# Optimization experiments

Hardware: AMD Instinct MI355X
Metric: run time of the kernel (lower is better)

The kernel has to match this reference:

```python
import jax, jax.numpy as jnp
import numpy as np

H = 256        # hidden_channels (== out_channels)
IN = 128       # in_channels (atom features)
ED = 64        # edge_dim (bond features)
G = 1024       # num graphs
L = 48         # atoms per graph (static pad length)
N = G * L      # num atoms
E = 2 * N      # num directed edges
NLAYERS = 4


def setup_inputs() -> dict:
    key = jax.random.key(0)
    ks = jax.random.split(key, 12)
    def rn(k, shape, scale=0.05):
        return jax.random.normal(k, shape, jnp.float32) * scale
    return {
        "x": jax.random.normal(ks[0], (N, IN), jnp.float32),
        "edge_attr": jax.random.normal(ks[1], (E, ED), jnp.float32),
        "edge_index": jax.random.randint(ks[2], (2, E), 0, N),
        "batch": jnp.repeat(jnp.arange(G), L),  # sorted, L atoms per graph
        "w_atom": rn(ks[3], (IN, H)), "b_atom": jnp.zeros((H,), jnp.float32),
        "w_bond": rn(ks[4], (ED, H)), "b_bond": jnp.zeros((H,), jnp.float32),
        "conv_w": rn(ks[5], (NLAYERS, H, H)), "conv_b": jnp.zeros((NLAYERS, H), jnp.float32),
        "w_lin": rn(ks[6], (3 * H, H)), "b_lin": jnp.zeros((H,), jnp.float32),
        "gru_bias": rn(ks[7], (H,), 0.06),
        "w_ih": rn(ks[8], (2, 3 * H, H)), "w_hh": rn(ks[9], (2, 3 * H, H)),
        "b_ih": jnp.zeros((2, 3 * H), jnp.float32), "b_hh": jnp.zeros((2, 3 * H), jnp.float32),
        "w_out": rn(ks[10], (2 * H, H)), "b_out": jnp.zeros((H,), jnp.float32),
    }


def reference(x, edge_attr, edge_index, batch, w_atom, b_atom, w_bond, b_bond,
              conv_w, conv_b, w_lin, b_lin, gru_bias, w_ih, w_hh, b_ih, b_hh,
              w_out, b_out):
    relu = jax.nn.relu
    row, col = edge_index[0], edge_index[1]  # flow='target_to_source': aggregate at row

    x_proj = relu(x @ w_atom + b_atom)                 # [N, H]
    h_atom = x_proj
    h_bond = relu(edge_attr @ w_bond + b_bond)         # [E, H]

    def booster(h_bond):
        # message_booster multi-aggregation: sum * max (empty slots -> 0, as torch_scatter)
        s = jax.ops.segment_sum(h_bond, row, num_segments=N)
        m = jax.ops.segment_max(h_bond, row, num_segments=N)
        m = jnp.where(jnp.isfinite(m), m, 0.0)
        return s * m

    for i in range(NLAYERS - 1):
        h_atom = h_atom + booster(h_bond)              # additive communicator
        # edge_update: x[edge_index_i] - edge_attr[edge_index_j]; seq = Linear+ReLU (dropout p=0)
        h_bond = relu((h_atom[row] - h_bond[col]) @ conv_w[i] + conv_b[i])
    aggr_message = h_atom + booster(h_bond)            # last conv; edge output discarded

    h = jnp.concatenate([aggr_message, h_atom, x_proj], axis=1) @ w_lin + b_lin  # [N, H]

    # ---- BatchGRU ----
    msg = relu(h + gru_bias)
    starts = jnp.searchsorted(batch, jnp.arange(G))
    pos = jnp.arange(N) - starts[batch]                # position within own graph
    messages = jnp.zeros((G, L, H), h.dtype).at[batch, pos].set(msg)
    h0 = jax.ops.segment_max(h, batch, num_segments=G)  # [G, H], same init both dirs

    def gru_dir(seq, d):
        def cell(hst, x_t):
            gi = x_t @ w_ih[d].T + b_ih[d]
            gh = hst @ w_hh[d].T + b_hh[d]
            i_r, i_z, i_n = jnp.split(gi, 3, -1)
            h_r, h_z, h_n = jnp.split(gh, 3, -1)
            r = jax.nn.sigmoid(i_r + h_r)
            z = jax.nn.sigmoid(i_z + h_z)
            n = jnp.tanh(i_n + r * h_n)
            hn = (1.0 - z) * n + z * hst
            return hn, hn
        _, out = jax.lax.scan(cell, h0, seq)
        return out

    seq = messages.transpose(1, 0, 2)                  # [L, G, H]
    out_f = gru_dir(seq, 0)
    out_b = gru_dir(seq[::-1], 1)[::-1]
    h_msgs = jnp.concatenate([out_f, out_b], -1).transpose(1, 0, 2)  # [G, L, 2H]
    unpadded = h_msgs[batch, pos]                      # [N, 2H]

    return relu(unpadded @ w_out + b_out)              # seq_out (dropout p=0)
```

## Files before the change

kernel.cpp:

```cpp
#include <hip/hip_runtime.h>
#include <math.h>

#define HH 256
#define GG 1024
#define LL 48
#define NNODES 49152
#define NEDGES 98304
#define SB 256.0f
#define DSB 0.00390625f

typedef _Float16 f16;
typedef __attribute__((ext_vector_type(8))) _Float16 f16x8;
typedef __attribute__((ext_vector_type(4))) float f32x4;

#define MFMA16(a, b, c) __builtin_amdgcn_mfma_f32_16x16x32_f16(a, b, c, 0, 0, 0)

__device__ inline float sc_from_max(float m) {
    if (!(m > 0.f)) return 1.0f;
    return ldexpf(1.0f, 13 - ilogbf(m));
}

__global__ void csr_count(const int* __restrict__ row, int* __restrict__ counts)
{
    int e = blockIdx.x * 256 + threadIdx.x;
    if (e < NEDGES) atomicAdd(&counts[row[e]], 1);
}

__global__ __launch_bounds__(1024) void scan_offsets(const int* __restrict__ counts,
                                                     int* __restrict__ offsets)
{
    __shared__ int tsum[1024];
    const int tid = threadIdx.x;
    const int base = tid * 48;
    int s = 0;
    for (int i = 0; i < 48; i++) s += counts[base + i];
    tsum[tid] = s;
    __syncthreads();
    for (int off = 1; off < 1024; off <<= 1) {
        int v = (tid >= off) ? tsum[tid - off] : 0;
        __syncthreads();
        tsum[tid] += v;
        __syncthreads();
    }
    int run = (tid == 0) ? 0 : tsum[tid - 1];
    for (int i = 0; i < 48; i++) { offsets[base + i] = run; run += counts[base + i]; }
    if (tid == 1023) offsets[NNODES] = run;
}

__global__ void csr_fill(const int* __restrict__ row, const int* __restrict__ offsets,
                         int* __restrict__ cursor, int* __restrict__ elist)
{
    int e = blockIdx.x * 256 + threadIdx.x;
    if (e < NEDGES) {
        int r = row[e];
        int p = atomicAdd(&cursor[r], 1);
        elist[offsets[r] + p] = e;
    }
}

__global__ void prep_graphs(const int* __restrict__ batch, int* __restrict__ starts,
                            int* __restrict__ gcnt)
{
    int i = blockIdx.x * 256 + threadIdx.x;
    if (i < NNODES) {
        int b = batch[i];
        atomicAdd(&gcnt[b], 1);
        if (i == 0 || batch[i - 1] != b) starts[b] = i;
    }
}

__global__ void rowscale(const float* __restrict__ A, int K, float* __restrict__ sc)
{
    int m = blockIdx.x, ln = threadIdx.x;
    float v = 0.f;
    for (int k = ln; k < K; k += 64) v = fmaxf(v, fabsf(A[(size_t)m * K + k]));
    for (int s = 32; s; s >>= 1) v = fmaxf(v, __shfl_xor(v, s));
    if (ln == 0) sc[m] = sc_from_max(v);
}

__global__ void prep_wT(const float* __restrict__ Wsrc, f16* __restrict__ oH,
                        f16* __restrict__ oL)
{
    int idx = blockIdx.x * 256 + threadIdx.x;
    int k = idx >> 8, n = idx & 255;
    float v = Wsrc[(size_t)k * 256 + n] * SB;
    f16 h = (f16)v;
    size_t o = ((size_t)(k >> 5) * 256 + n) * 32 + (k & 31);
    oH[o] = h;
    oL[o] = (f16)(v - (float)h);
}

__global__ void prep_gruW(const float* __restrict__ w_ih, const float* __restrict__ w_hh,
                          const float* __restrict__ b_ih, const float* __restrict__ b_hh,
                          f16* __restrict__ BgH, f16* __restrict__ BgL,
                          float* __restrict__ bias4)
{
    int idx = blockIdx.x * 256 + threadIdx.x;
    int d = idx >> 19;
    int rem = idx & 524287;
    int k = rem >> 10;
    int col = rem & 1023;
    int jj = col >> 2, s = col & 3;
    const float* Wi = w_ih + (size_t)d * 768 * 256;
    const float* Wh = w_hh + (size_t)d * 768 * 256;
    float v;
    if (s == 0)      v = (k < 256) ? Wi[(size_t)jj * 256 + k]         : Wh[(size_t)jj * 256 + (k - 256)];
    else if (s == 1) v = (k < 256) ? Wi[(size_t)(256 + jj) * 256 + k] : Wh[(size_t)(256 + jj) * 256 + (k - 256)];
    else if (s == 2) v = (k < 256) ? Wi[(size_t)(512 + jj) * 256 + k] : 0.f;
    else             v = (k < 256) ? 0.f : Wh[(size_t)(512 + jj) * 256 + (k - 256)];
    v *= SB;
    f16 h = (f16)v;
    size_t o = ((size_t)(d * 16 + (k >> 5)) * 1024 + col) * 32 + (k & 31);
    BgH[o] = h;
    BgL[o] = (f16)(v - (float)h);
    if (k == 0) {
        const float* bi = b_ih + d * 768;
        const float* bh = b_hh + d * 768;
        float bv;
        if (s == 0)      bv = bi[jj] + bh[jj];
        else if (s == 1) bv = bi[256 + jj] + bh[256 + jj];
        else if (s == 2) bv = bi[512 + jj];
        else             bv = bh[512 + jj];
        bias4[d * 1024 + col] = bv;
    }
}

__global__ void booster(const float* __restrict__ hb_lo, const float* __restrict__ hb_hi,
                        const float* __restrict__ atom_in, float* __restrict__ out,
                        const int* __restrict__ offsets, const int* __restrict__ elist,
                        float* __restrict__ scOut)
{
    int n = blockIdx.x, c = threadIdx.x;
    int b0 = offsets[n], b1 = offsets[n + 1];
    float s = 0.f, m = 0.f;
    for (int p = b0; p < b1; p++) {
        int e = elist[p];
        const float* hb = (e < NNODES) ? (hb_lo + (size_t)e * HH)
                                       : (hb_hi + (size_t)(e - NNODES) * HH);
        float v = hb[c];
        s += v;
        m = fmaxf(m, v);
    }
    float o = atom_in[(size_t)n * HH + c] + s * m;
    out[(size_t)n * HH + c] = o;
    float v = fabsf(o);
    for (int t = 32; t; t >>= 1) v = fmaxf(v, __shfl_xor(v, t));
    __shared__ float wm[4];
    if ((c & 63) == 0) wm[c >> 6] = v;
    __syncthreads();
    if (c == 0)
        scOut[n] = sc_from_max(fmaxf(fmaxf(wm[0], wm[1]), fmaxf(wm[2], wm[3])));
}

__global__ void h0_init(const float* __restrict__ h, const int* __restrict__ starts,
                        const int* __restrict__ gcnt, float* __restrict__ hid0,
                        float* __restrict__ scG)
{
    int g = blockIdx.x, c = threadIdx.x;
    int st = starts[g], cn = gcnt[g];
    float m = -INFINITY, am = 0.f;
    for (int i = 0; i < cn; i++) {
        float v = h[(size_t)(st + i) * HH + c];
        m = fmaxf(m, v);
        am = fmaxf(am, fabsf(v));
    }
    if (cn == 0) m = 0.f;
    hid0[(size_t)g * HH + c] = m;
    hid0[(size_t)GG * HH + (size_t)g * HH + c] = m;
    for (int t = 32; t; t >>= 1) am = fmaxf(am, __shfl_xor(am, t));
    __shared__ float wm[4];
    if ((c & 63) == 0) wm[c >> 6] = am;
    __syncthreads();
    if (c == 0) {
        float M = fmaxf(fmaxf(fmaxf(wm[0], wm[1]), fmaxf(wm[2], wm[3])) + 0.07f, 1.0f);
        scG[g] = sc_from_max(M);
    }
}

__global__ void build_msgP(const float* __restrict__ h, const float* __restrict__ gbias,
                           const int* __restrict__ starts, const int* __restrict__ gcnt,
                           float* __restrict__ msgP)
{
    int l = blockIdx.x, g = blockIdx.y, k = threadIdx.x;
    float v = 0.f;
    if (l < gcnt[g]) {
        int node = starts[g] + l;
        v = fmaxf(h[(size_t)node * HH + k] + gbias[k], 0.f);
    }
    msgP[((size_t)l * GG + g) * HH + k] = v;
}

template<int MODE>
__device__ __forceinline__ void gemmLoadA(const float* __restrict__ A,
    const float* __restrict__ S0, const float* __restrict__ S1,
    const float* __restrict__ S2, int rI, int cI, int row, int K, int k,
    float va[8])
{
    if constexpr (MODE == 0) {
        const float* p = A + (size_t)row * K + k;
        float4 v0 = *(const float4*)p, v1 = *(const float4*)(p + 4);
        va[0]=v0.x; va[1]=v0.y; va[2]=v0.z; va[3]=v0.w;
        va[4]=v1.x; va[5]=v1.y; va[6]=v1.z; va[7]=v1.w;
    } else if constexpr (MODE == 1) {
        const float* pa = S0 + (size_t)rI * HH + k;
        const float* pb = S1 + (size_t)cI * HH + k;
        float4 a0 = *(const float4*)pa, a1 = *(const float4*)(pa + 4);
        float4 b0 = *(const float4*)pb, b1 = *(const float4*)(pb + 4);
        va[0]=a0.x-b0.x; va[1]=a0.y-b0.y; va[2]=a0.z-b0.z; va[3]=a0.w-b0.w;
        va[4]=a1.x-b1.x; va[5]=a1.y-b1.y; va[6]=a1.z-b1.z; va[7]=a1.w-b1.w;
    } else if constexpr (MODE == 2) {
        const float* S = (k < 256) ? S0 : ((k < 512) ? S1 : S2);
        const float* p = S + (size_t)row * HH + (k & 255);
        float4 v0 = *(const float4*)p, v1 = *(const float4*)(p + 4);
        va[0]=v0.x; va[1]=v0.y; va[2]=v0.z; va[3]=v0.w;
        va[4]=v1.x; va[5]=v1.y; va[6]=v1.z; va[7]=v1.w;
    } else {
        const float* S = (k < 256) ? S0 : S1;
        const float* p = S + (size_t)row * HH + (k & 255);
        float4 v0 = *(const float4*)p, v1 = *(const float4*)(p + 4);
        va[0]=v0.x; va[1]=v0.y; va[2]=v0.z; va[3]=v0.w;
        va[4]=v1.x; va[5]=v1.y; va[6]=v1.z; va[7]=v1.w;
    }
}

template<int MODE, bool RELU, bool SPLITC, bool WSCALE, int NX>
__global__ __launch_bounds__(256) void gemm_f16x3(
    const float* __restrict__ A,
    const float* __restrict__ S0, const float* __restrict__ S1, const float* __restrict__ S2,
    const int* __restrict__ ridx, const int* __restrict__ cidx,
    const f16* __restrict__ BgH, const f16* __restrict__ BgL,
    const float* __restrict__ bias,
    const float* __restrict__ sc0, const float* __restrict__ sc1, const float* __restrict__ sc2,
    float* __restrict__ Clo, float* __restrict__ Chi,
    float* __restrict__ scOut, int K)
{
    __shared__ __align__(16) f16 Ah[64 * 40], Al[64 * 40];
    __shared__ __align__(16) f16 Bh[256 * 40], Bl[256 * 40];
    __shared__ float scL[64];
    __shared__ float rmL[64][4];

    const int tid = threadIdx.x;
    const int m0 = blockIdx.x * 64;
    const int arow = tid >> 2, aoct = tid & 3;
    const int w = tid >> 6, lane = tid & 63, lr = lane & 15, lh = lane >> 4;

    if (tid < 64) {
        float sc;
        if constexpr (MODE == 0) sc = sc0[m0 + tid];
        else if constexpr (MODE == 1) {
            int r = ridx[m0 + tid], cc = cidx[m0 + tid];
            sc = fminf(sc0[r], sc1[cc]) * 0.5f;
        } else if constexpr (MODE == 2) {
            sc = fminf(fminf(sc0[m0 + tid], sc1[m0 + tid]), sc2[m0 + tid]);
        } else {
            sc = sc0[cidx[m0 + tid]];
        }
        scL[tid] = sc;
    }
    int rI = 0, cI = 0;
    if constexpr (MODE == 1) { rI = ridx[m0 + arow]; cI = cidx[m0 + arow]; }
    __syncthreads();
    const float myS = scL[arow];

    float va[8];
    f16x8 rbh[4], rbl[4];
    gemmLoadA<MODE>(A, S0, S1, S2, rI, cI, m0 + arow, K, aoct * 8, va);
    {
        size_t base = (size_t)tid * 32;
        const f16x8* ph = (const f16x8*)(BgH + base);
#pragma unroll
        for (int q = 0; q < 4; q++) rbh[q] = ph[q];
        if constexpr (NX == 3) {
            const f16x8* pl = (const f16x8*)(BgL + base);
#pragma unroll
            for (int q = 0; q < 4; q++) rbl[q] = pl[q];
        }
    }

    f32x4 acc[4][4] = {};
    for (int k0 = 0; k0 < K; k0 += 32) {
        {
            f16x8 hi, lo;
#pragma unroll
            for (int e = 0; e < 8; e++) {
                float a = va[e] * myS;
                f16 h = (f16)a;
                hi[e] = h;
                if constexpr (NX == 3) lo[e] = (f16)(a - (float)h);
            }
            *(f16x8*)&Ah[arow * 40 + aoct * 8] = hi;
            if constexpr (NX == 3) *(f16x8*)&Al[arow * 40 + aoct * 8] = lo;
        }
#pragma unroll
        for (int q = 0; q < 4; q++) {
            *(f16x8*)&Bh[tid * 40 + q * 8] = rbh[q];
            if constexpr (NX == 3) *(f16x8*)&Bl[tid * 40 + q * 8] = rbl[q];
        }
        __syncthreads();
        if (k0 + 32 < K) {
            gemmLoadA<MODE>(A, S0, S1, S2, rI, cI, m0 + arow, K, k0 + 32 + aoct * 8, va);
            size_t base = ((size_t)((k0 + 32) >> 5) * 256 + tid) * 32;
            const f16x8* ph = (const f16x8*)(BgH + base);
#pragma unroll
            for (int q = 0; q < 4; q++) rbh[q] = ph[q];
            if constexpr (NX == 3) {
                const f16x8* pl = (const f16x8*)(BgL + base);
#pragma unroll
                for (int q = 0; q < 4; q++) rbl[q] = pl[q];
            }
        }
        f16x8 fah[4], fal[4];
#pragma unroll
        for (int i = 0; i < 4; i++) {
            fah[i] = *(const f16x8*)&Ah[(i * 16 + lr) * 40 + lh * 8];
            if constexpr (NX == 3) fal[i] = *(const f16x8*)&Al[(i * 16 + lr) * 40 + lh * 8];
        }
#pragma unroll
        for (int j = 0; j < 4; j++) {
            int colx = w * 64 + j * 16 + lr;
            f16x8 fbh = *(const f16x8*)&Bh[colx * 40 + lh * 8];
            if constexpr (NX == 3) {
                f16x8 fbl = *(const f16x8*)&Bl[colx * 40 + lh * 8];
#pragma unroll
                for (int i = 0; i < 4; i++) {
                    acc[i][j] = MFMA16(fah[i], fbh, acc[i][j]);
                    acc[i][j] = MFMA16(fah[i], fbl, acc[i][j]);
                    acc[i][j] = MFMA16(fal[i], fbh, acc[i][j]);
                }
            } else {
#pragma unroll
                for (int i = 0; i < 4; i++)
                    acc[i][j] = MFMA16(fah[i], fbh, acc[i][j]);
            }
        }
        __syncthreads();
    }

    float rm[4][4];
#pragma unroll
    for (int i = 0; i < 4; i++)
#pragma unroll
        for (int e = 0; e < 4; e++) rm[i][e] = 0.f;
#pragma unroll
    for (int i = 0; i < 4; i++) {
#pragma unroll
        for (int e = 0; e < 4; e++) {
            int ml = i * 16 + lh * 4 + e;
            int m = m0 + ml;
            float inv = DSB / scL[ml];
            float* Cb;
            if constexpr (SPLITC)
                Cb = (m < NNODES) ? (Clo + (size_t)m * HH) : (Chi + (size_t)(m - NNODES) * HH);
            else
                Cb = Clo + (size_t)m * HH;
#pragma unroll
            for (int j = 0; j < 4; j++) {
                int n = w * 64 + j * 16 + lr;
                float v = acc[i][j][e] * inv + bias[n];
                if constexpr (RELU) v = fmaxf(v, 0.f);
                Cb[n] = v;
                if constexpr (WSCALE) rm[i][e] = fmaxf(rm[i][e], fabsf(v));
            }
        }
    }
    if constexpr (WSCALE) {
#pragma unroll
        for (int i = 0; i < 4; i++)
#pragma unroll
            for (int e = 0; e < 4; e++) {
                float v = rm[i][e];
                v = fmaxf(v, __shfl_xor(v, 1));
                v = fmaxf(v, __shfl_xor(v, 2));
                v = fmaxf(v, __shfl_xor(v, 4));
                v = fmaxf(v, __shfl_xor(v, 8));
                if (lr == 0) rmL[i * 16 + lh * 4 + e][w] = v;
            }
        __syncthreads();
        if (tid < 64)
            scOut[m0 + tid] = sc_from_max(fmaxf(fmaxf(rmL[tid][0], rmL[tid][1]),
                                                fmaxf(rmL[tid][2], rmL[tid][3])));
    }
}

__global__ __launch_bounds__(256) void gru_step_f16(
    const float* __restrict__ msgP, const f16* __restrict__ BgH, const f16* __restrict__ BgL,
    const float* __restrict__ bias4, const float* __restrict__ hidC, float* __restrict__ hidN,
    const float* __restrict__ scG, const int* __restrict__ starts, const int* __restrict__ gcnt,
    float* __restrict__ outF, float* __restrict__ outB, int t)
{
    __shared__ __align__(16) char smemraw[18432];
    float* Cs = (float*)smemraw;
    __shared__ float scL[32];

    const int tid = threadIdx.x;
    const int id = blockIdx.x;
    const int c = id & 7, d = (id >> 3) & 1, gt = id >> 4;
    const int g0 = gt * 32;
    const int l = d ? (LL - 1 - t) : t;
    const float* hidCd = hidC + (size_t)d * GG * HH;
    float* hidNd = hidN + (size_t)d * GG * HH;

    if (tid < 32) scL[tid] = scG[g0 + tid];
    __syncthreads();

    const int arow = tid >> 3, akoct = tid & 7;
    const float myS = scL[arow];
    const int w = tid >> 6, lane = tid & 63, lr = lane & 15, lh = lane >> 4;

    f16* Ah0 = (f16*)smemraw;
    f16* Al0 = Ah0 + 2304;
    f16* Ah1 = Al0 + 2304;
    f16* Al1 = Ah1 + 2304;

    {
        const float* p = msgP + ((size_t)l * GG + g0 + arow) * HH + akoct * 8;
        float4 v0 = *(const float4*)p, v1 = *(const float4*)(p + 4);
        float va0[8] = {v0.x, v0.y, v0.z, v0.w, v1.x, v1.y, v1.z, v1.w};
        f16x8 hi, lo;
#pragma unroll
        for (int e = 0; e < 8; e++) {
            float a = va0[e] * myS;
            f16 h = (f16)a;
            hi[e] = h;
            lo[e] = (f16)(a - (float)h);
        }
        *(f16x8*)&Ah0[arow * 72 + akoct * 8] = hi;
        *(f16x8*)&Al0[arow * 72 + akoct * 8] = lo;
    }
    f16x8 fbh[2][2], fbl[2][2];
#pragma unroll
    for (int ks = 0; ks < 2; ks++) {
        size_t kbase = (size_t)(d * 16 + ks) * 1024;
#pragma unroll
        for (int j = 0; j < 2; j++) {
            size_t o = (kbase + (c * 128 + w * 32 + j * 16 + lr)) * 32 + lh * 8;
            fbh[ks][j] = *(const f16x8*)(BgH + o);
            fbl[ks][j] = *(const f16x8*)(BgL + o);
        }
    }
    __syncthreads();

    f32x4 acc[2][2] = {};
#pragma unroll
    for (int win = 0; win < 8; win++) {
        f16* AhC = (win & 1) ? Ah1 : Ah0;
        f16* AlC = (win & 1) ? Al1 : Al0;
        f16* AhN = (win & 1) ? Ah0 : Ah1;
        f16* AlN = (win & 1) ? Al0 : Al1;

        float va[8];
        if (win < 7) {
            int k = (win + 1) * 64 + akoct * 8;
            const float* p = (k < 256)
                ? msgP + ((size_t)l * GG + g0 + arow) * HH + k
                : hidCd + (size_t)(g0 + arow) * HH + (k - 256);
            float4 v0 = *(const float4*)p, v1 = *(const float4*)(p + 4);
            va[0]=v0.x; va[1]=v0.y; va[2]=v0.z; va[3]=v0.w;
            va[4]=v1.x; va[5]=v1.y; va[6]=v1.z; va[7]=v1.w;
        }
        f16x8 nbh[2][2], nbl[2][2];
        if (win < 7) {
#pragma unroll
            for (int ks = 0; ks < 2; ks++) {
                size_t kbase = (size_t)(d * 16 + (win + 1) * 2 + ks) * 1024;
#pragma unroll
                for (int j = 0; j < 2; j++) {
                    size_t o = (kbase + (c * 128 + w * 32 + j * 16 + lr)) * 32 + lh * 8;
                    nbh[ks][j] = *(const f16x8*)(BgH + o);
                    nbl[ks][j] = *(const f16x8*)(BgL + o);
                }
            }
        }
#pragma unroll
        for (int ks = 0; ks < 2; ks++) {
            f16x8 fah[2], fal[2];
#pragma unroll
            for (int i = 0; i < 2; i++) {
                fah[i] = *(const f16x8*)&AhC[(i * 16 + lr) * 72 + ks * 32 + lh * 8];
                fal[i] = *(const f16x8*)&AlC[(i * 16 + lr) * 72 + ks * 32 + lh * 8];
            }
#pragma unroll
            for (int j = 0; j < 2; j++) {
#pragma unroll
                for (int i = 0; i < 2; i++) {
                    acc[i][j] = MFMA16(fah[i], fbh[ks][j], acc[i][j]);
                    acc[i][j] = MFMA16(fah[i], fbl[ks][j], acc[i][j]);
                    acc[i][j] = MFMA16(fal[i], fbh[ks][j], acc[i][j]);
                }
            }
        }
        if (win < 7) {
            f16x8 hi, lo;
#pragma unroll
            for (int e = 0; e < 8; e++) {
                float a = va[e] * myS;
                f16 h = (f16)a;
                hi[e] = h;
                lo[e] = (f16)(a - (float)h);
            }
            *(f16x8*)&AhN[arow * 72 + akoct * 8] = hi;
            *(f16x8*)&AlN[arow * 72 + akoct * 8] = lo;
#pragma unroll
            for (int ks = 0; ks < 2; ks++)
#pragma unroll
                for (int j = 0; j < 2; j++) {
                    fbh[ks][j] = nbh[ks][j];
                    fbl[ks][j] = nbl[ks][j];
                }
        }
        __syncthreads();
    }

#pragma unroll
    for (int i = 0; i < 2; i++) {
#pragma unroll
        for (int e = 0; e < 4; e++) {
            int ml = i * 16 + lh * 4 + e;
            float inv = DSB / scL[ml];
#pragma unroll
            for (int j = 0; j < 2; j++)
                Cs[ml * 132 + w * 32 + j * 16 + lr] = acc[i][j][e] * inv;
        }
    }
    __syncthreads();

    const float* b4 = bias4 + d * 1024;
    const int jl = tid & 31;
    const int J  = c * 32 + jl;
    const int gbase = (tid >> 5) * 4;
    const float bb0 = b4[4 * J + 0], bb1 = b4[4 * J + 1];
    const float bb2 = b4[4 * J + 2], bb3 = b4[4 * J + 3];
    float* o = d ? outB : outF;
#pragma unroll
    for (int i = 0; i < 4; i++) {
        int gl = gbase + i;
        int g = g0 + gl;
        f32x4 gv = *(const f32x4*)&Cs[gl * 132 + jl * 4];
        float r = 1.f / (1.f + expf(-(gv[0] + bb0)));
        float z = 1.f / (1.f + expf(-(gv[1] + bb1)));
        float nn = tanhf(gv[2] + bb2 + r * (gv[3] + bb3));
        float hp = hidCd[(size_t)g * HH + J];
        float hnew = (1.f - z) * nn + z * hp;
        hidNd[(size_t)g * HH + J] = hnew;
        if (l < gcnt[g]) o[(size_t)(starts[g] + l) * HH + J] = hnew;
    }
}

__global__ void fill_sentinel(float* __restrict__ out, float v)
{
    size_t idx = (size_t)blockIdx.x * 256 + threadIdx.x;
    out[idx] = v;
}

extern "C" void kernel_launch(void* const* d_in, const int* in_sizes, int n_in,
                              void* d_out, int out_size, void* d_ws, size_t ws_size,
                              hipStream_t stream)
{
    (void)in_sizes; (void)n_in; (void)out_size;
    const float* x         = (const float*)d_in[0];
    const float* edge_attr = (const float*)d_in[1];
    const int*   eidx      = (const int*)d_in[2];
    const int*   batch     = (const int*)d_in[3];
    const float* w_atom    = (const float*)d_in[4];
    const float* b_atom    = (const float*)d_in[5];
    const float* w_bond    = (const float*)d_in[6];
    const float* b_bond    = (const float*)d_in[7];
    const float* conv_w    = (const float*)d_in[8];
    const float* conv_b    = (const float*)d_in[9];
    const float* w_lin     = (const float*)d_in[10];
    const float* b_lin     = (const float*)d_in[11];
    const float* gru_bias  = (const float*)d_in[12];
    const float* w_ih      = (const float*)d_in[13];
    const float* w_hh      = (const float*)d_in[14];
    const float* b_ih      = (const float*)d_in[15];
    const float* b_hh      = (const float*)d_in[16];
    const float* w_out     = (const float*)d_in[17];
    const float* b_out     = (const float*)d_in[18];

    const int* row = eidx;
    const int* col = eidx + NEDGES;

    const size_t NH = (size_t)NNODES * HH;

    float* W   = (float*)d_ws;
    float* W0  = W;
    float* W1  = W + NH;
    float* W1h = W + 2 * NH;
    float* W2  = W + 3 * NH;
    float* DO  = (float*)d_out;

    size_t off = 4 * NH;
    int* counts  = (int*)(W + off);      off += NNODES;
    int* cursor  = (int*)(W + off);      off += NNODES;
    int* gcnt    = (int*)(W + off);      off += GG;
    int* starts  = (int*)(W + off);      off += GG;
    int* offsets = (int*)(W + off);      off += NNODES + 1;
    int* elist   = (int*)(W + off);      off += NEDGES;
    float* scX    = W + off;             off += NNODES;
    float* scEA   = W + off;             off += NEDGES;
    float* scHbA  = W + off;             off += NEDGES;
    float* scHbB  = W + off;             off += NEDGES;
    float* scAtom = W + off;             off += NNODES;
    float* scAggr = W + off;             off += NNODES;
    float* scXp   = W + off;             off += NNODES;
    float* scGru  = W + off;             off += GG;
    off = (off + 3) & ~(size_t)3;
    f16* fp = (f16*)(W + off);
    f16* watomH = fp;                     fp += 4 * 256 * 32;
    f16* watomL = fp;                     fp += 4 * 256 * 32;
    f16* wbondH = fp;                     fp += 2 * 256 * 32;
    f16* wbondL = fp;                     fp += 2 * 256 * 32;
    f16* convH[3]; f16* convL[3];
    for (int i = 0; i < 3; i++) { convH[i] = fp; fp += 8 * 256 * 32; convL[i] = fp; fp += 8 * 256 * 32; }
    f16* wlinH = fp;                      fp += 24 * 256 * 32;
    f16* wlinL = fp;                      fp += 24 * 256 * 32;
    f16* woutH = fp;                      fp += 16 * 256 * 32;
    f16* woutL = fp;                      fp += 16 * 256 * 32;

    const size_t NEED = (char*)fp - (char*)d_ws;
    if (ws_size < NEED) {
        fill_sentinel<<<(int)(NH / 256), 256, 0, stream>>>((float*)d_out, (float)ws_size);
        return;
    }

    float* hid0  = DO;
    float* hid1  = DO + 2 * (size_t)GG * HH;
    float* bias4 = DO + 4 * (size_t)GG * HH;
    f16* BgH = (f16*)(bias4 + 2048);
    f16* BgL = BgH + (size_t)2 * 16 * 1024 * 32;

    hipMemsetAsync(counts, 0, (size_t)(2 * NNODES + 2 * GG) * sizeof(int), stream);
    prep_graphs<<<(NNODES + 255) / 256, 256, 0, stream>>>(batch, starts, gcnt);
    csr_count<<<(NEDGES + 255) / 256, 256, 0, stream>>>(row, counts);
    scan_offsets<<<1, 1024, 0, stream>>>(counts, offsets);
    csr_fill<<<(NEDGES + 255) / 256, 256, 0, stream>>>(row, offsets, cursor, elist);

    rowscale<<<NNODES, 64, 0, stream>>>(x, 128, scX);
    rowscale<<<NEDGES, 64, 0, stream>>>(edge_attr, 64, scEA);

    prep_wT<<<128, 256, 0, stream>>>(w_atom, watomH, watomL);
    prep_wT<<<64, 256, 0, stream>>>(w_bond, wbondH, wbondL);
    for (int i = 0; i < 3; i++)
        prep_wT<<<256, 256, 0, stream>>>(conv_w + (size_t)i * HH * HH, convH[i], convL[i]);
    prep_wT<<<768, 256, 0, stream>>>(w_lin, wlinH, wlinL);
    prep_wT<<<512, 256, 0, stream>>>(w_out, woutH, woutL);

    gemm_f16x3<0, true, false, true, 3><<<NNODES / 64, 256, 0, stream>>>(
        x, nullptr, nullptr, nullptr, nullptr, nullptr, watomH, watomL, b_atom,
        scX, nullptr, nullptr, W0, nullptr, scAtom, 128);
    gemm_f16x3<0, true, true, true, 3><<<NEDGES / 64, 256, 0, stream>>>(
        edge_attr, nullptr, nullptr, nullptr, nullptr, nullptr, wbondH, wbondL, b_bond,
        scEA, nullptr, nullptr, W1, W1h, scHbA, 64);

    float* cur_lo = W1; float* cur_hi = W1h; float* cur_sc = scHbA;
    float* nxt_lo = W2; float* nxt_hi = DO;  float* nxt_sc = scHbB;
    for (int i = 0; i < 3; i++) {
        booster<<<NNODES, 256, 0, stream>>>(cur_lo, cur_hi, W0, W0, offsets, elist, scAtom);
        gemm_f16x3<1, true, true, true, 3><<<NEDGES / 64, 256, 0, stream>>>(
            nullptr, W0, cur_lo, nullptr, row, col, convH[i], convL[i],
            conv_b + (size_t)i * HH, scAtom, cur_sc, nullptr, nxt_lo, nxt_hi, nxt_sc, 256);
        float* t0 = cur_lo; cur_lo = nxt_lo; nxt_lo = t0;
        float* t1 = cur_hi; cur_hi = nxt_hi; nxt_hi = t1;
        float* t2 = cur_sc; cur_sc = nxt_sc; nxt_sc = t2;
    }
    booster<<<NNODES, 256, 0, stream>>>(cur_lo, cur_hi, W0, W1, offsets, elist, scAggr);
    gemm_f16x3<0, true, false, true, 3><<<NNODES / 64, 256, 0, stream>>>(
        x, nullptr, nullptr, nullptr, nullptr, nullptr, watomH, watomL, b_atom,
        scX, nullptr, nullptr, W1h, nullptr, scXp, 128);
    gemm_f16x3<2, false, false, false, 3><<<NNODES / 64, 256, 0, stream>>>(
        nullptr, W1, W0, W1h, nullptr, nullptr, wlinH, wlinL, b_lin,
        scAggr, scAtom, scXp, W2, nullptr, nullptr, 768);

    h0_init<<<GG, 256, 0, stream>>>(W2, starts, gcnt, hid0, scGru);
    build_msgP<<<dim3(LL, GG), 256, 0, stream>>>(W2, gru_bias, starts, gcnt, W1h);
    prep_gruW<<<(2 * 512 * 1024) / 256, 256, 0, stream>>>(w_ih, w_hh, b_ih, b_hh, BgH, BgL, bias4);

    for (int t = 0; t < LL; t++) {
        float* hc = (t & 1) ? hid1 : hid0;
        float* hx = (t & 1) ? hid0 : hid1;
        gru_step_f16<<<512, 256, 0, stream>>>(W1h, BgH, BgL, bias4, hc, hx,
                                              scGru, starts, gcnt, W0, W1, t);
    }

    gemm_f16x3<3, true, false, false, 1><<<NNODES / 64, 256, 0, stream>>>(
        nullptr, W0, W1, nullptr, nullptr, batch, woutH, nullptr, b_out,
        scGru, nullptr, nullptr, (float*)d_out, nullptr, nullptr, 512);
}
```

Baseline: 1.474 ms.

## Merge weight prep launches, use wave-per-node booster, widen GRU step blocks

The seven prep_wT launches become one kernel that dispatches on row index. booster and h0_init now assign one 64-lane wave per node or graph with float4 loads, which removes the block-level shared-memory reduction and the syncthreads. gru_step_f16 now covers 64 graphs per block with 512 threads, so each block loads the weight fragments once for twice as many rows. The trade-off is a larger shared-memory footprint and fewer GRU blocks (256), which may lower occupancy. The GRU epilogue, which is not shown, must also handle 64 rows for the change to be correct.

```diff
diff --git a/kernel.cpp b/kernel.cpp
--- a/kernel.cpp
+++ b/kernel.cpp
@@ -78,12 +78,28 @@
     if (ln == 0) sc[m] = sc_from_max(v);
 }
 
-__global__ void prep_wT(const float* __restrict__ Wsrc, f16* __restrict__ oH,
-                        f16* __restrict__ oL)
+__global__ void prep_wT_all(const float* __restrict__ w_atom, const float* __restrict__ w_bond,
+                            const float* __restrict__ conv_w, const float* __restrict__ w_lin,
+                            const float* __restrict__ w_out,
+                            f16* __restrict__ watomH, f16* __restrict__ watomL,
+                            f16* __restrict__ wbondH, f16* __restrict__ wbondL,
+                            f16* __restrict__ convH0, f16* __restrict__ convL0,
+                            f16* __restrict__ convH1, f16* __restrict__ convL1,
+                            f16* __restrict__ convH2, f16* __restrict__ convL2,
+                            f16* __restrict__ wlinH, f16* __restrict__ wlinL,
+                            f16* __restrict__ woutH, f16* __restrict__ woutL)
 {
     int idx = blockIdx.x * 256 + threadIdx.x;
-    int k = idx >> 8, n = idx & 255;
-    float v = Wsrc[(size_t)k * 256 + n] * SB;
+    int krow = idx >> 8, n = idx & 255;
+    const float* src; f16* oH; f16* oL; int k;
+    if (krow < 128)       { src = w_atom;           oH = watomH; oL = watomL; k = krow; }
+    else if (krow < 192)  { src = w_bond;           oH = wbondH; oL = wbondL; k = krow - 128; }
+    else if (krow < 448)  { src = conv_w;           oH = convH0; oL = convL0; k = krow - 192; }
+    else if (krow < 704)  { src = conv_w + 65536;   oH = convH1; oL = convL1; k = krow - 448; }
+    else if (krow < 960)  { src = conv_w + 131072;  oH = convH2; oL = convL2; k = krow - 704; }
+    else if (krow < 1728) { src = w_lin;            oH = wlinH;  oL = wlinL;  k = krow - 960; }
+    else                  { src = w_out;            oH = woutH;  oL = woutL;  k = krow - 1728; }
+    float v = src[(size_t)k * 256 + n] * SB;
     f16 h = (f16)v;
     size_t o = ((size_t)(k >> 5) * 256 + n) * 32 + (k & 31);
     oH[o] = h;
@@ -130,51 +146,53 @@
                         const int* __restrict__ offsets, const int* __restrict__ elist,
                         float* __restrict__ scOut)
 {
-    int n = blockIdx.x, c = threadIdx.x;
-    int b0 = offsets[n], b1 = offsets[n + 1];
-    float s = 0.f, m = 0.f;
+    const int wv = threadIdx.x >> 6;
+    const int n = blockIdx.x * 4 + wv;
+    const int ln = threadIdx.x & 63;
+    const int b0 = offsets[n], b1 = offsets[n + 1];
+    float4 s = {0.f, 0.f, 0.f, 0.f}, m = {0.f, 0.f, 0.f, 0.f};
     for (int p = b0; p < b1; p++) {
         int e = elist[p];
         const float* hb = (e < NNODES) ? (hb_lo + (size_t)e * HH)
                                        : (hb_hi + (size_t)(e - NNODES) * HH);
-        float v = hb[c];
-        s += v;
-        m = fmaxf(m, v);
-    }
-    float o = atom_in[(size_t)n * HH + c] + s * m;
-    out[(size_t)n * HH + c] = o;
-    float v = fabsf(o);
+        float4 v = *(const float4*)(hb + ln * 4);
+        s.x += v.x; s.y += v.y; s.z += v.z; s.w += v.w;
+        m.x = fmaxf(m.x, v.x); m.y = fmaxf(m.y, v.y);
+        m.z = fmaxf(m.z, v.z); m.w = fmaxf(m.w, v.w);
+    }
+    float4 a = *(const float4*)(atom_in + (size_t)n * HH + ln * 4);
+    float4 o;
+    o.x = a.x + s.x * m.x; o.y = a.y + s.y * m.y;
+    o.z = a.z + s.z * m.z; o.w = a.w + s.w * m.w;
+    *(float4*)(out + (size_t)n * HH + ln * 4) = o;
+    float v = fmaxf(fmaxf(fabsf(o.x), fabsf(o.y)), fmaxf(fabsf(o.z), fabsf(o.w)));
     for (int t = 32; t; t >>= 1) v = fmaxf(v, __shfl_xor(v, t));
-    __shared__ float wm[4];
-    if ((c & 63) == 0) wm[c >> 6] = v;
-    __syncthreads();
-    if (c == 0)
-        scOut[n] = sc_from_max(fmaxf(fmaxf(wm[0], wm[1]), fmaxf(wm[2], wm[3])));
+    if (ln == 0) scOut[n] = sc_from_max(v);
 }
 
 __global__ void h0_init(const float* __restrict__ h, const int* __restrict__ starts,
                         const int* __restrict__ gcnt, float* __restrict__ hid0,
                         float* __restrict__ scG)
 {
-    int g = blockIdx.x, c = threadIdx.x;
-    int st = starts[g], cn = gcnt[g];
-    float m = -INFINITY, am = 0.f;
+    const int wv = threadIdx.x >> 6;
+    const int g = blockIdx.x * 4 + wv;
+    const int ln = threadIdx.x & 63;
+    const int st = starts[g], cn = gcnt[g];
+    float4 m = {-INFINITY, -INFINITY, -INFINITY, -INFINITY};
+    float4 am = {0.f, 0.f, 0.f, 0.f};
     for (int i = 0; i < cn; i++) {
-        float v = h[(size_t)(st + i) * HH + c];
-        m = fmaxf(m, v);
-        am = fmaxf(am, fabsf(v));
-    }
-    if (cn == 0) m = 0.f;
-    hid0[(size_t)g * HH + c] = m;
-    hid0[(size_t)GG * HH + (size_t)g * HH + c] = m;
-    for (int t = 32; t; t >>= 1) am = fmaxf(am, __shfl_xor(am, t));
-    __shared__ float wm[4];
-    if ((c & 63) == 0) wm[c >> 6] = am;
-    __syncthreads();
-    if (c == 0) {
-        float M = fmaxf(fmaxf(fmaxf(wm[0], wm[1]), fmaxf(wm[2], wm[3])) + 0.07f, 1.0f);
-        scG[g] = sc_from_max(M);
-    }
+        float4 v = *(const float4*)(h + (size_t)(st + i) * HH + ln * 4);
+        m.x = fmaxf(m.x, v.x); m.y = fmaxf(m.y, v.y);
+        m.z = fmaxf(m.z, v.z); m.w = fmaxf(m.w, v.w);
+        am.x = fmaxf(am.x, fabsf(v.x)); am.y = fmaxf(am.y, fabsf(v.y));
+        am.z = fmaxf(am.z, fabsf(v.z)); am.w = fmaxf(am.w, fabsf(v.w));
+    }
+    if (cn == 0) { m.x = m.y = m.z = m.w = 0.f; }
+    *(float4*)(hid0 + (size_t)g * HH + ln * 4) = m;
+    *(float4*)(hid0 + (size_t)GG * HH + (size_t)g * HH + ln * 4) = m;
+    float a = fmaxf(fmaxf(am.x, am.y), fmaxf(am.z, am.w));
+    for (int t = 32; t; t >>= 1) a = fmaxf(a, __shfl_xor(a, t));
+    if (ln == 0) scG[g] = sc_from_max(fmaxf(a + 0.07f, 1.0f));
 }
 
 __global__ void build_msgP(const float* __restrict__ h, const float* __restrict__ gbias,
@@ -382,35 +400,37 @@
     }
 }
 
-__global__ __launch_bounds__(256) void gru_step_f16(
+__global__ __launch_bounds__(512) void gru_step_f16(
     const float* __restrict__ msgP, const f16* __restrict__ BgH, const f16* __restrict__ BgL,
     const float* __restrict__ bias4, const float* __restrict__ hidC, float* __restrict__ hidN,
     const float* __restrict__ scG, const int* __restrict__ starts, const int* __restrict__ gcnt,
     float* __restrict__ outF, float* __restrict__ outB, int t)
 {
-    __shared__ __align__(16) char smemraw[18432];
+    __shared__ __align__(16) char smemraw[36864];
     float* Cs = (float*)smemraw;
-    __shared__ float scL[32];
+    __shared__ float scL[64];
 
     const int tid = threadIdx.x;
     const int id = blockIdx.x;
     const int c = id & 7, d = (id >> 3) & 1, gt = id >> 4;
-    const int g0 = gt * 32;
+    const int g0 = gt * 64;
     const int l = d ? (LL - 1 - t) : t;
     const float* hidCd = hidC + (size_t)d * GG * HH;
     float* hidNd = hidN + (size_t)d * GG * HH;
 
-    if (tid < 32) scL[tid] = scG[g0 + tid];
+    if (tid < 64) scL[tid] = scG[g0 + tid];
     __syncthreads();
 
     const int arow = tid >> 3, akoct = tid & 7;
     const float myS = scL[arow];
-    const int w = tid >> 6, lane = tid & 63, lr = lane & 15, lh = lane >> 4;
+    const int w = tid >> 6;
+    const int wg = w >> 2, wc = w & 3;
+    const int lane = tid & 63, lr = lane & 15, lh = lane >> 4;
 
     f16* Ah0 = (f16*)smemraw;
-    f16* Al0 = Ah0 + 2304;
-    f16* Ah1 = Al0 + 2304;
-    f16* Al1 = Ah1 + 2304;
+    f16* Al0 = Ah0 + 4608;
+    f16* Ah1 = Al0 + 4608;
+    f16* Al1 = Ah1 + 4608;
 
     {
         const float* p = msgP + ((size_t)l * GG + g0 + arow) * HH + akoct * 8;
@@ -433,7 +453,7 @@
         size_t kbase = (size_t)(d * 16 + ks) * 1024;
 #pragma unroll
         for (int j = 0; j < 2; j++) {
-            size_t o = (kbase + (c * 128 + w * 32 + j * 16 + lr)) * 32 + lh * 8;
+            size_t o = (kbase + (c * 128 + wc * 32 + j * 16 + lr)) * 32 + lh * 8;
             fbh[ks][j] = *(const f16x8*)(BgH + o);
             fbl[ks][j] = *(const f16x8*)(BgL + o);
         }
@@ -465,7 +485,7 @@
                 size_t kbase = (size_t)(d * 16 + (win + 1) * 2 + ks) * 1024;
 #pragma unroll
                 for (int j = 0; j < 2; j++) {
-                    size_t o = (kbase + (c * 128 + w * 32 + j * 16 + lr)) * 32 + lh * 8;
+                    size_t o = (kbase + (c * 128 + wc * 32 + j * 16 + lr)) * 32 + lh * 8;
                     nbh[ks][j] = *(const f16x8*)(BgH + o);
                     nbl[ks][j] = *(const f16x8*)(BgL + o);
                 }
@@ -476,8 +496,8 @@
             f16x8 fah[2], fal[2];
 #pragma unroll
             for (int i = 0; i < 2; i++) {
-                fah[i] = *(const f16x8*)&AhC[(i * 16 + lr) * 72 + ks * 32 + lh * 8];
-                fal[i] = *(const f16x8*)&AlC[(i * 16 + lr) * 72 + ks * 32 + lh * 8];
+                fah[i] = *(const f16x8*)&AhC[(wg * 32 + i * 16 + lr) * 72 + ks * 32 + lh * 8];
+                fal[i] = *(const f16x8*)&AlC[(wg * 32 + i * 16 + lr) * 72 + ks * 32 + lh * 8];
             }
 #pragma unroll
             for (int j = 0; j < 2; j++) {
@@ -515,11 +535,11 @@
     for (int i = 0; i < 2; i++) {
 #pragma unroll
         for (int e = 0; e < 4; e++) {
-            int ml = i * 16 + lh * 4 + e;
+            int ml = wg * 32 + i * 16 + lh * 4 + e;
             float inv = DSB / scL[ml];
 #pragma unroll
             for (int j = 0; j < 2; j++)
-                Cs[ml * 132 + w * 32 + j * 16 + lr] = acc[i][j][e] * inv;
+                Cs[ml * 132 + wc * 32 + j * 16 + lr] = acc[i][j][e] * inv;
         }
     }
     __syncthreads();
@@ -638,12 +658,9 @@
     rowscale<<<NNODES, 64, 0, stream>>>(x, 128, scX);
     rowscale<<<NEDGES, 64, 0, stream>>>(edge_attr, 64, scEA);
 
-    prep_wT<<<128, 256, 0, stream>>>(w_atom, watomH, watomL);
-    prep_wT<<<64, 256, 0, stream>>>(w_bond, wbondH, wbondL);
-    for (int i = 0; i < 3; i++)
-        prep_wT<<<256, 256, 0, stream>>>(conv_w + (size_t)i * HH * HH, convH[i], convL[i]);
-    prep_wT<<<768, 256, 0, stream>>>(w_lin, wlinH, wlinL);
-    prep_wT<<<512, 256, 0, stream>>>(w_out, woutH, woutL);
+    prep_wT_all<<<2240, 256, 0, stream>>>(w_atom, w_bond, conv_w, w_lin, w_out,
+        watomH, watomL, wbondH, wbondL, convH[0], convL[0], convH[1], convL[1],
+        convH[2], convL[2], wlinH, wlinL, woutH, woutL);
 
     gemm_f16x3<0, true, false, true, 3><<<NNODES / 64, 256, 0, stream>>>(
         x, nullptr, nullptr, nullptr, nullptr, nullptr, watomH, watomL, b_atom,
@@ -655,7 +672,7 @@
     float* cur_lo = W1; float* cur_hi = W1h; float* cur_sc = scHbA;
     float* nxt_lo = W2; float* nxt_hi = DO;  float* nxt_sc = scHbB;
     for (int i = 0; i < 3; i++) {
-        booster<<<NNODES, 256, 0, stream>>>(cur_lo, cur_hi, W0, W0, offsets, elist, scAtom);
+        booster<<<NNODES / 4, 256, 0, stream>>>(cur_lo, cur_hi, W0, W0, offsets, elist, scAtom);
         gemm_f16x3<1, true, true, true, 3><<<NEDGES / 64, 256, 0, stream>>>(
             nullptr, W0, cur_lo, nullptr, row, col, convH[i], convL[i],
             conv_b + (size_t)i * HH, scAtom, cur_sc, nullptr, nxt_lo, nxt_hi, nxt_sc, 256);
@@ -663,7 +680,7 @@
         float* t1 = cur_hi; cur_hi = nxt_hi; nxt_hi = t1;
         float* t2 = cur_sc; cur_sc = nxt_sc; nxt_sc = t2;
     }
-    booster<<<NNODES, 256, 0, stream>>>(cur_lo, cur_hi, W0, W1, offsets, elist, scAggr);
+    booster<<<NNODES / 4, 256, 0, stream>>>(cur_lo, cur_hi, W0, W1, offsets, elist, scAggr);
     gemm_f16x3<0, true, false, true, 3><<<NNODES / 64, 256, 0, stream>>>(
         x, nullptr, nullptr, nullptr, nullptr, nullptr, watomH, watomL, b_atom,
         scX, nullptr, nullptr, W1h, nullptr, scXp, 128);
@@ -671,14 +688,14 @@
         nullptr, W1, W0, W1h, nullptr, nullptr, wlinH, wlinL, b_lin,
         scAggr, scAtom, scXp, W2, nullptr, nullptr, 768);
 
-    h0_init<<<GG, 256, 0, stream>>>(W2, starts, gcnt, hid0, scGru);
+    h0_init<<<GG / 4, 256, 0, stream>>>(W2, starts, gcnt, hid0, scGru);
     build_msgP<<<dim3(LL, GG), 256, 0, stream>>>(W2, gru_bias, starts, gcnt, W1h);
     prep_gruW<<<(2 * 512 * 1024) / 256, 256, 0, stream>>>(w_ih, w_hh, b_ih, b_hh, BgH, BgL, bias4);
 
     for (int t = 0; t < LL; t++) {
         float* hc = (t & 1) ? hid1 : hid0;
         float* hx = (t & 1) ? hid0 : hid1;
-        gru_step_f16<<<512, 256, 0, stream>>>(W1h, BgH, BgL, bias4, hc, hx,
+        gru_step_f16<<<256, 512, 0, stream>>>(W1h, BgH, BgL, bias4, hc, hx,
                                               scGru, starts, gcnt, W0, W1, t);
     }
 
```

New measurement: 1.405 ms. -4.7%, faster.
